# Kernel tuning notes

Measured on AMD Instinct MI355X. Metric: run time of the kernel, lower is better.

## Reference

```python
import jax, jax.numpy as jnp
import numpy as np
import math

IN_FEATURES = 4096
OUT_FEATURES = 4096
P = max(IN_FEATURES, OUT_FEATURES)   # total_permutations
D = min(IN_FEATURES, OUT_FEATURES)   # diag_length
SPARSITY = 0.1
K = math.ceil(int((1.0 - SPARSITY) * IN_FEATURES * OUT_FEATURES) / D)  # 3687
ALPHA_LR = 0.01
NUM_ITER = 50


def sparse_soft_topk_mask_dykstra(alpha, k, l, num_iter):
    """Dykstra projection of alpha/l onto {0<=m<=1, sum(m)=k} (soft top-k mask)."""
    s = alpha / l
    n = s.shape[0]
    p0 = jnp.zeros_like(s)
    q0 = jnp.zeros_like(s)

    def body(carry, _):
        x, p, q = carry
        # project x+p onto hyperplane sum = k
        t = x + p
        y = t + (k - jnp.sum(t)) / n
        p = t - y
        # project y+q onto box [0, 1]
        u = y + q
        x_new = jnp.clip(u, 0.0, 1.0)
        q = u - x_new
        return (x_new, p, q), None

    (x, _, _), _ = jax.lax.scan(body, (s, p0, q0), None, length=num_iter)
    return x  # last projection is onto the box -> exact zeros / ones


def compute_weight(V, alpha):
    a = sparse_soft_topk_mask_dykstra(alpha, K, ALPHA_LR, NUM_ITER)  # (P,)
    vals = a[:, None] * V                                             # (P, D)
    i = jnp.arange(P)[:, None]
    j = jnp.arange(D)[None, :]
    if OUT_FEATURES >= IN_FEATURES:
        # pseudo-diagonal i: rows shifted by i, column j scaled by V[i, j]
        rows = (i + j) % OUT_FEATURES
        cols = jnp.broadcast_to(j, (P, D))
    else:
        # row r scaled by V[i, r], columns shifted by i
        rows = jnp.broadcast_to(j, (P, D))
        cols = (i + j) % IN_FEATURES
    W = jnp.zeros((OUT_FEATURES, IN_FEATURES), V.dtype)
    W = W.at[rows.reshape(-1), cols.reshape(-1)].add(vals.reshape(-1))
    return W


def setup_inputs() -> dict:
    key = jax.random.key(0)
    k1, k2 = jax.random.split(key)
    # kaiming_uniform_(a=sqrt(5)) over fan_in = D -> bound = sqrt(1/D)
    bound = 1.0 / np.sqrt(D)
    V = jax.random.uniform(k1, (P, D), jnp.float32, -bound, bound)
    alpha = jnp.ones((P,), jnp.float32) / IN_FEATURES
    x = jax.random.normal(k2, (512, IN_FEATURES), jnp.float32)
    return {"x": x, "V": V, "alpha": alpha}


def reference(x, V, alpha):
    W = compute_weight(V, alpha)  # (out, in)
    return x @ W.T                # F.linear(x, W)
```

## Files before the change

### kernel.cpp

```cpp
#include <hip/hip_runtime.h>
#include <hip/hip_bf16.h>
#include <stdint.h>

#define PDIM 4096
#define KSEL 3687.0f
#define NITER 50

typedef unsigned short ushort_t;
typedef __attribute__((ext_vector_type(8))) __bf16 bf16x8;
typedef __attribute__((ext_vector_type(4))) float f32x4;

typedef __attribute__((address_space(3))) void lds_void;
typedef __attribute__((address_space(1))) const void glob_void;

__device__ __forceinline__ ushort_t f32_to_bf16_rne(float f) {
  union { float f; uint32_t u; } v; v.f = f;
  uint32_t r = 0x7FFFu + ((v.u >> 16) & 1u);
  return (ushort_t)((v.u + r) >> 16);
}

__device__ __forceinline__ float bf16_to_f32(ushort_t h) {
  union { uint32_t u; float f; } v; v.u = ((uint32_t)h) << 16;
  return v.f;
}

__device__ __forceinline__ void async_cp16(const void* g, void* l) {
  __builtin_amdgcn_global_load_lds((glob_void*)g, (lds_void*)l, 16, 0, 0);
}

__global__ __launch_bounds__(256) void prep_kernel(
    const float* __restrict__ alpha, float* __restrict__ a_out,
    const float* __restrict__ x, ushort_t* __restrict__ Xb, int n4) {
  if (blockIdx.x != 0) {
    const int i = (blockIdx.x - 1) * 256 + threadIdx.x;
    if (i < n4) {
      const float4 v = ((const float4*)x)[i];
      ushort4 o;
      o.x = f32_to_bf16_rne(v.x);
      o.y = f32_to_bf16_rne(v.y);
      o.z = f32_to_bf16_rne(v.z);
      o.w = f32_to_bf16_rne(v.w);
      ((ushort4*)Xb)[i] = o;
    }
    return;
  }
  __shared__ float red[8];
  const int tid = threadIdx.x;
  const int lane = tid & 63;
  const int wv = tid >> 6;
  float xx[16], q[16];
  float p = 0.0f;
#pragma unroll
  for (int i = 0; i < 16; ++i) {
    xx[i] = alpha[i * 256 + tid] * 100.0f;
    q[i] = 0.0f;
  }
  for (int it = 0; it < NITER; ++it) {
    float t[16];
    float loc = 0.0f;
#pragma unroll
    for (int i = 0; i < 16; ++i) { t[i] = xx[i] + p; loc += t[i]; }
#pragma unroll
    for (int off = 32; off > 0; off >>= 1) loc += __shfl_down(loc, off, 64);
    const int slot = (it & 1) * 4;
    if (lane == 0) red[slot + wv] = loc;
    __syncthreads();
    const float tot = red[slot] + red[slot + 1] + red[slot + 2] + red[slot + 3];
    const float corr = (KSEL - tot) * (1.0f / 4096.0f);
    p = -corr;
#pragma unroll
    for (int i = 0; i < 16; ++i) {
      const float y = t[i] + corr;
      const float u = y + q[i];
      const float xn = fminf(fmaxf(u, 0.0f), 1.0f);
      q[i] = u - xn;
      xx[i] = xn;
    }
  }
#pragma unroll
  for (int i = 0; i < 16; ++i) a_out[i * 256 + tid] = xx[i];
}

__global__ __launch_bounds__(256) void wmat_kernel(
    const float* __restrict__ V, const float* __restrict__ a,
    ushort_t* __restrict__ Wb) {
  __shared__ float vt[192][67];
  const int t = threadIdx.x;
  const int r0 = blockIdx.x * 128;
  const int c0 = blockIdx.y * 64;
  const int dbase = (r0 - c0 - 63 + 2 * PDIM) & (PDIM - 1);
  const int csub = (t & 15) * 4;
  const int rsub = t >> 4;
#pragma unroll
  for (int i = 0; i < 12; ++i) {
    const int ld = i * 16 + rsub;
    const int d = (dbase + ld) & (PDIM - 1);
    const float av = a[d];
    const float4 vv = *(const float4*)(V + (size_t)d * PDIM + c0 + csub);
    vt[ld][csub + 0] = av * vv.x;
    vt[ld][csub + 1] = av * vv.y;
    vt[ld][csub + 2] = av * vv.z;
    vt[ld][csub + 3] = av * vv.w;
  }
  __syncthreads();
#pragma unroll
  for (int k = 0; k < 4; ++k) {
    const int ry = (t >> 3) + k * 32;
    const int cb = (t & 7) * 8;
    ushort_t pk[8];
#pragma unroll
    for (int j = 0; j < 8; ++j) {
      const int c = cb + j;
      pk[j] = f32_to_bf16_rne(vt[ry - c + 63][c]);
    }
    *(uint4*)(Wb + (size_t)(r0 + ry) * PDIM + c0 + cb) = *(const uint4*)pk;
  }
}

__global__ __launch_bounds__(256, 3) void gemm_kernel(
    const ushort_t* __restrict__ Xb, const ushort_t* __restrict__ Wb,
    ushort_t* __restrict__ par) {
  constexpr int Kdim = 4096, KQ = 1024;
  __shared__ __align__(16) ushort_t As[128 * 64];
  __shared__ __align__(16) ushort_t Bs[128 * 64];
  const int tid = threadIdx.x;
  const int lane = tid & 63;
  const int w = tid >> 6;
  const int l15 = lane & 15;
  const int quad = lane >> 4;
  const int z = blockIdx.x;
  const int nblk = blockIdx.y;
  const int mblk = blockIdx.z;
  const int m0 = mblk * 128;
  const int n0 = nblk * 128;
  const int kbase = z * KQ;
  const int arow = lane >> 3;
  const int aslot = lane & 7;

  f32x4 acc[8][2];
#pragma unroll
  for (int mt = 0; mt < 8; ++mt)
#pragma unroll
    for (int nt = 0; nt < 2; ++nt) acc[mt][nt] = (f32x4){0.f, 0.f, 0.f, 0.f};

  for (int it = 0; it < KQ / 64; ++it) {
    const int k0 = kbase + it * 64;
#pragma unroll
    for (int s = w; s < 16; s += 4) {
      const int row = s * 8 + arow;
      const int j = aslot ^ (row & 7);
      async_cp16(Xb + (size_t)(m0 + row) * Kdim + k0 + j * 8,
                 (char*)As + (size_t)s * 1024);
      async_cp16(Wb + (size_t)(n0 + row) * Kdim + k0 + j * 8,
                 (char*)Bs + (size_t)s * 1024);
    }
    __syncthreads();
#pragma unroll
    for (int kk = 0; kk < 64; kk += 32) {
      const int cj = (kk >> 3) + quad;
      bf16x8 bfv[2];
#pragma unroll
      for (int nt = 0; nt < 2; ++nt) {
        const int row = w * 32 + nt * 16 + l15;
        bfv[nt] = *(const bf16x8*)&Bs[(row * 8 + (cj ^ (row & 7))) * 8];
      }
#pragma unroll
      for (int mt = 0; mt < 8; ++mt) {
        const int row = mt * 16 + l15;
        const bf16x8 af = *(const bf16x8*)&As[(row * 8 + (cj ^ (row & 7))) * 8];
        acc[mt][0] = __builtin_amdgcn_mfma_f32_16x16x32_bf16(af, bfv[0],
                                                             acc[mt][0], 0, 0, 0);
        acc[mt][1] = __builtin_amdgcn_mfma_f32_16x16x32_bf16(af, bfv[1],
                                                             acc[mt][1], 0, 0, 0);
      }
    }
    __syncthreads();
  }
  const int tile = nblk * 4 + mblk;
  ushort_t* pbase = par + ((size_t)z * 128 + tile) * 16384;
#pragma unroll
  for (int mt = 0; mt < 8; ++mt) {
#pragma unroll
    for (int nt = 0; nt < 2; ++nt) {
      const int slot = mt * 2 + nt;
      ushort4 o;
      o.x = f32_to_bf16_rne(acc[mt][nt][0]);
      o.y = f32_to_bf16_rne(acc[mt][nt][1]);
      o.z = f32_to_bf16_rne(acc[mt][nt][2]);
      o.w = f32_to_bf16_rne(acc[mt][nt][3]);
      *(ushort4*)(pbase + (size_t)(slot * 256 + tid) * 4) = o;
    }
  }
}

__global__ __launch_bounds__(256) void combine_kernel(
    const ushort_t* __restrict__ par, float* __restrict__ out) {
  const int tile = blockIdx.x >> 2;
  const int qh = blockIdx.x & 3;
  const int nblk = tile >> 2;
  const int mblk = tile & 3;
  const int m0 = mblk * 128;
  const int n0 = nblk * 128;
  const int tid = threadIdx.x;
  const int lane = tid & 63;
  const int w = tid >> 6;
  const int l15 = lane & 15;
  const int quad = lane >> 4;
#pragma unroll
  for (int ss = 0; ss < 4; ++ss) {
    const int slot = qh * 4 + ss;
    float s0 = 0.f, s1 = 0.f, s2 = 0.f, s3 = 0.f;
#pragma unroll
    for (int z = 0; z < 4; ++z) {
      const ushort4 v = *(const ushort4*)(par +
          ((size_t)z * 128 + tile) * 16384 + (size_t)(slot * 256 + tid) * 4);
      s0 += bf16_to_f32(v.x);
      s1 += bf16_to_f32(v.y);
      s2 += bf16_to_f32(v.z);
      s3 += bf16_to_f32(v.w);
    }
    const int mt = slot >> 1;
    const int nt = slot & 1;
    const int mb = m0 + mt * 16 + quad * 4;
    const int n = n0 + w * 32 + nt * 16 + l15;
    out[(size_t)(mb + 0) * PDIM + n] = s0;
    out[(size_t)(mb + 1) * PDIM + n] = s1;
    out[(size_t)(mb + 2) * PDIM + n] = s2;
    out[(size_t)(mb + 3) * PDIM + n] = s3;
  }
}

extern "C" void kernel_launch(void* const* d_in, const int* in_sizes, int n_in,
                              void* d_out, int out_size, void* d_ws,
                              size_t ws_size, hipStream_t stream) {
  const float* x = (const float*)d_in[0];
  const float* V = (const float*)d_in[1];
  const float* alpha = (const float*)d_in[2];
  float* out = (float*)d_out;
  const int M = in_sizes[0] / PDIM;

  float* a_mask = (float*)d_ws;
  ushort_t* Xb = (ushort_t*)((char*)d_ws + 16 * 1024);
  ushort_t* Wb = Xb + (size_t)M * PDIM;
  ushort_t* par = Wb + (size_t)PDIM * PDIM;

  const int n4x = (M * PDIM) / 4;
  prep_kernel<<<1 + (n4x + 255) / 256, 256, 0, stream>>>(alpha, a_mask, x, Xb,
                                                         n4x);
  wmat_kernel<<<dim3(PDIM / 128, PDIM / 64), 256, 0, stream>>>(V, a_mask, Wb);
  gemm_kernel<<<dim3(4, PDIM / 128, M / 128), 256, 0, stream>>>(Xb, Wb, par);
  combine_kernel<<<512, 256, 0, stream>>>(par, out);
}
```

Baseline: 157.1 us.

## Fuse prep, weight build, GEMM and combine into one cooperative kernel

Replaces the four separate launches with a single cooperative mega-kernel that runs the mask projection, x conversion, weight materialization, split-K GEMM and combine as phases separated by grid-wide syncs. The aim is to remove inter-kernel launch gaps and tail effects. The weight-build phase now stages bf16 values in LDS instead of fp32, which shrinks shared memory. This requires all 512 blocks to be co-resident, and it keeps the fallback path of separate launches in case the cooperative launch fails.

Result: slower. 327.2 us (+108.3%).

```diff
diff --git a/kernel.cpp b/kernel.cpp
--- a/kernel.cpp
+++ b/kernel.cpp
@@ -1,10 +1,15 @@
 #include <hip/hip_runtime.h>
+#include <hip/hip_cooperative_groups.h>
 #include <hip/hip_bf16.h>
 #include <stdint.h>
+
+namespace cg = cooperative_groups;
 
 #define PDIM 4096
 #define KSEL 3687.0f
 #define NITER 50
+#define MDIM 512
+#define N4X ((MDIM * PDIM) / 4)
 
 typedef unsigned short ushort_t;
 typedef __attribute__((ext_vector_type(8))) __bf16 bf16x8;
@@ -26,6 +31,216 @@
 
 __device__ __forceinline__ void async_cp16(const void* g, void* l) {
   __builtin_amdgcn_global_load_lds((glob_void*)g, (lds_void*)l, 16, 0, 0);
+}
+
+__global__ __launch_bounds__(256) void mega_kernel(
+    const float* __restrict__ alpha, float* __restrict__ a_mask,
+    const float* __restrict__ x, ushort_t* __restrict__ Xb,
+    const float* __restrict__ V, ushort_t* __restrict__ Wb,
+    ushort_t* __restrict__ par, float* __restrict__ out) {
+  cg::grid_group grid = cg::this_grid();
+  __shared__ __align__(16) union {
+    ushort_t vt[192 * 70];
+    struct { ushort_t As[128 * 64]; ushort_t Bs[128 * 64]; } g;
+    float red[8];
+  } sm;
+
+  const int bid = blockIdx.x;
+  const int tid = threadIdx.x;
+  const int lane = tid & 63;
+  const int w = tid >> 6;
+  const int l15 = lane & 15;
+  const int quad = lane >> 4;
+
+  if (bid == 0) {
+    const int wv = tid >> 6;
+    float xx[16], q[16];
+    float p = 0.0f;
+#pragma unroll
+    for (int i = 0; i < 16; ++i) {
+      xx[i] = alpha[i * 256 + tid] * 100.0f;
+      q[i] = 0.0f;
+    }
+    for (int it = 0; it < NITER; ++it) {
+      float t[16];
+      float loc = 0.0f;
+#pragma unroll
+      for (int i = 0; i < 16; ++i) { t[i] = xx[i] + p; loc += t[i]; }
+#pragma unroll
+      for (int off = 32; off > 0; off >>= 1) loc += __shfl_down(loc, off, 64);
+      const int slot = (it & 1) * 4;
+      if (lane == 0) sm.red[slot + wv] = loc;
+      __syncthreads();
+      const float tot =
+          sm.red[slot] + sm.red[slot + 1] + sm.red[slot + 2] + sm.red[slot + 3];
+      const float corr = (KSEL - tot) * (1.0f / 4096.0f);
+      p = -corr;
+#pragma unroll
+      for (int i = 0; i < 16; ++i) {
+        const float y = t[i] + corr;
+        const float u = y + q[i];
+        const float xn = fminf(fmaxf(u, 0.0f), 1.0f);
+        q[i] = u - xn;
+        xx[i] = xn;
+      }
+    }
+#pragma unroll
+    for (int i = 0; i < 16; ++i) a_mask[i * 256 + tid] = xx[i];
+  } else {
+    const int stride = 511 * 256;
+    for (int i = (bid - 1) * 256 + tid; i < N4X; i += stride) {
+      const float4 v = ((const float4*)x)[i];
+      ushort4 o;
+      o.x = f32_to_bf16_rne(v.x);
+      o.y = f32_to_bf16_rne(v.y);
+      o.z = f32_to_bf16_rne(v.z);
+      o.w = f32_to_bf16_rne(v.w);
+      ((ushort4*)Xb)[i] = o;
+    }
+  }
+  grid.sync();
+
+  {
+    const int csub = (tid & 15) * 4;
+    const int rsub = tid >> 4;
+#pragma unroll 1
+    for (int j = 0; j < 4; ++j) {
+      const int tn = bid * 4 + j;
+      const int r0 = (tn & 31) * 128;
+      const int c0 = (tn >> 5) * 64;
+      const int dbase = (r0 - c0 - 63 + 2 * PDIM) & (PDIM - 1);
+#pragma unroll
+      for (int i = 0; i < 12; ++i) {
+        const int ld = i * 16 + rsub;
+        const int d = (dbase + ld) & (PDIM - 1);
+        const float av = a_mask[d];
+        const float4 vv = *(const float4*)(V + (size_t)d * PDIM + c0 + csub);
+        ushort_t* row = &sm.vt[ld * 70 + csub];
+        ushort2 lo, hi;
+        lo.x = f32_to_bf16_rne(av * vv.x);
+        lo.y = f32_to_bf16_rne(av * vv.y);
+        hi.x = f32_to_bf16_rne(av * vv.z);
+        hi.y = f32_to_bf16_rne(av * vv.w);
+        *(ushort2*)(row) = lo;
+        *(ushort2*)(row + 2) = hi;
+      }
+      __syncthreads();
+#pragma unroll
+      for (int k = 0; k < 4; ++k) {
+        const int ry = (tid >> 3) + k * 32;
+        const int cb = (tid & 7) * 8;
+        ushort_t pk[8];
+#pragma unroll
+        for (int jj = 0; jj < 8; ++jj) {
+          const int c = cb + jj;
+          pk[jj] = sm.vt[(ry - c + 63) * 70 + c];
+        }
+        *(uint4*)(Wb + (size_t)(r0 + ry) * PDIM + c0 + cb) = *(const uint4*)pk;
+      }
+      __syncthreads();
+    }
+  }
+  grid.sync();
+
+  {
+    constexpr int Kdim = 4096, KQ = 1024;
+    const int z = bid & 3;
+    const int nblk = (bid >> 2) & 31;
+    const int mblk = bid >> 7;
+    const int m0 = mblk * 128;
+    const int n0 = nblk * 128;
+    const int kbase = z * KQ;
+    const int arow = lane >> 3;
+    const int aslot = lane & 7;
+
+    f32x4 acc[8][2];
+#pragma unroll
+    for (int mt = 0; mt < 8; ++mt)
+#pragma unroll
+      for (int nt = 0; nt < 2; ++nt) acc[mt][nt] = (f32x4){0.f, 0.f, 0.f, 0.f};
+
+    for (int it = 0; it < KQ / 64; ++it) {
+      const int k0 = kbase + it * 64;
+#pragma unroll
+      for (int s = w; s < 16; s += 4) {
+        const int row = s * 8 + arow;
+        const int j = aslot ^ (row & 7);
+        async_cp16(Xb + (size_t)(m0 + row) * Kdim + k0 + j * 8,
+                   (char*)sm.g.As + (size_t)s * 1024);
+        async_cp16(Wb + (size_t)(n0 + row) * Kdim + k0 + j * 8,
+                   (char*)sm.g.Bs + (size_t)s * 1024);
+      }
+      __syncthreads();
+#pragma unroll
+      for (int kk = 0; kk < 64; kk += 32) {
+        const int cj = (kk >> 3) + quad;
+        bf16x8 bfv[2];
+#pragma unroll
+        for (int nt = 0; nt < 2; ++nt) {
+          const int row = w * 32 + nt * 16 + l15;
+          bfv[nt] = *(const bf16x8*)&sm.g.Bs[(row * 8 + (cj ^ (row & 7))) * 8];
+        }
+#pragma unroll
+        for (int mt = 0; mt < 8; ++mt) {
+          const int row = mt * 16 + l15;
+          const bf16x8 af =
+              *(const bf16x8*)&sm.g.As[(row * 8 + (cj ^ (row & 7))) * 8];
+          acc[mt][0] = __builtin_amdgcn_mfma_f32_16x16x32_bf16(
+              af, bfv[0], acc[mt][0], 0, 0, 0);
+          acc[mt][1] = __builtin_amdgcn_mfma_f32_16x16x32_bf16(
+              af, bfv[1], acc[mt][1], 0, 0, 0);
+        }
+      }
+      __syncthreads();
+    }
+    const int tile = nblk * 4 + mblk;
+    ushort_t* pbase = par + ((size_t)z * 128 + tile) * 16384;
+#pragma unroll
+    for (int mt = 0; mt < 8; ++mt) {
+#pragma unroll
+      for (int nt = 0; nt < 2; ++nt) {
+        const int slot = mt * 2 + nt;
+        ushort4 o;
+        o.x = f32_to_bf16_rne(acc[mt][nt][0]);
+        o.y = f32_to_bf16_rne(acc[mt][nt][1]);
+        o.z = f32_to_bf16_rne(acc[mt][nt][2]);
+        o.w = f32_to_bf16_rne(acc[mt][nt][3]);
+        *(ushort4*)(pbase + (size_t)(slot * 256 + tid) * 4) = o;
+      }
+    }
+  }
+  grid.sync();
+
+  {
+    const int tile = bid >> 2;
+    const int qh = bid & 3;
+    const int nblk = tile >> 2;
+    const int mblk = tile & 3;
+    const int m0 = mblk * 128;
+    const int n0 = nblk * 128;
+#pragma unroll
+    for (int ss = 0; ss < 4; ++ss) {
+      const int slot = qh * 4 + ss;
+      float s0 = 0.f, s1 = 0.f, s2 = 0.f, s3 = 0.f;
+#pragma unroll
+      for (int z = 0; z < 4; ++z) {
+        const ushort4 v = *(const ushort4*)(par +
+            ((size_t)z * 128 + tile) * 16384 + (size_t)(slot * 256 + tid) * 4);
+        s0 += bf16_to_f32(v.x);
+        s1 += bf16_to_f32(v.y);
+        s2 += bf16_to_f32(v.z);
+        s3 += bf16_to_f32(v.w);
+      }
+      const int mt = slot >> 1;
+      const int nt = slot & 1;
+      const int mb = m0 + mt * 16 + quad * 4;
+      const int n = n0 + w * 32 + nt * 16 + l15;
+      out[(size_t)(mb + 0) * PDIM + n] = s0;
+      out[(size_t)(mb + 1) * PDIM + n] = s1;
+      out[(size_t)(mb + 2) * PDIM + n] = s2;
+      out[(size_t)(mb + 3) * PDIM + n] = s3;
+    }
+  }
 }
 
 __global__ __launch_bounds__(256) void prep_kernel(
@@ -237,17 +452,24 @@
   const float* V = (const float*)d_in[1];
   const float* alpha = (const float*)d_in[2];
   float* out = (float*)d_out;
-  const int M = in_sizes[0] / PDIM;
 
   float* a_mask = (float*)d_ws;
   ushort_t* Xb = (ushort_t*)((char*)d_ws + 16 * 1024);
-  ushort_t* Wb = Xb + (size_t)M * PDIM;
+  ushort_t* Wb = Xb + (size_t)MDIM * PDIM;
   ushort_t* par = Wb + (size_t)PDIM * PDIM;
 
-  const int n4x = (M * PDIM) / 4;
-  prep_kernel<<<1 + (n4x + 255) / 256, 256, 0, stream>>>(alpha, a_mask, x, Xb,
-                                                         n4x);
-  wmat_kernel<<<dim3(PDIM / 128, PDIM / 64), 256, 0, stream>>>(V, a_mask, Wb);
-  gemm_kernel<<<dim3(4, PDIM / 128, M / 128), 256, 0, stream>>>(Xb, Wb, par);
-  combine_kernel<<<512, 256, 0, stream>>>(par, out);
-}
+  void* args[] = {(void*)&alpha, (void*)&a_mask, (void*)&x,   (void*)&Xb,
+                  (void*)&V,     (void*)&Wb,     (void*)&par, (void*)&out};
+  hipError_t err = hipLaunchCooperativeKernel(
+      (const void*)mega_kernel, dim3(512), dim3(256), args, 0, stream);
+  if (err != hipSuccess) {
+    const int n4x = N4X;
+    prep_kernel<<<1 + (n4x + 255) / 256, 256, 0, stream>>>(alpha, a_mask, x,
+                                                           Xb, n4x);
+    wmat_kernel<<<dim3(PDIM / 128, PDIM / 64), 256, 0, stream>>>(V, a_mask,
+                                                                 Wb);
+    gemm_kernel<<<dim3(4, PDIM / 128, MDIM / 128), 256, 0, stream>>>(Xb, Wb,
+                                                                     par);
+    combine_kernel<<<512, 256, 0, stream>>>(par, out);
+  }
+}
```
